# Optimization experiments

Measured on AMD Instinct MI355X. Metric: run time of the kernel, lower is better.

Reference implementation:

```python
import jax, jax.numpy as jnp
import numpy as np

ALPHA = 0.9  # membrane leak / decay


def setup_inputs() -> dict:
    key = jax.random.key(0)
    ks = jax.random.split(key, 6)
    T, B, D, H = 512, 64, 256, 256
    inputs = jax.random.normal(ks[0], (T, B, D), dtype=jnp.float32)
    spike0 = jax.random.uniform(ks[1], (B, H), dtype=jnp.float32)  # initial state['spike']
    v0 = jnp.zeros((B, H), dtype=jnp.float32)                      # initial membrane potential
    W_in = jax.random.normal(ks[2], (D, H), dtype=jnp.float32) * (1.0 / np.sqrt(D))
    W_rec = jax.random.normal(ks[3], (H, H), dtype=jnp.float32) * (1.0 / np.sqrt(H))
    W_out = jax.random.normal(ks[4], (H, H), dtype=jnp.float32) * (1.0 / np.sqrt(H))
    b = jnp.zeros((H,), dtype=jnp.float32)
    return {"inputs": inputs, "spike0": spike0, "v0": v0,
            "W_in": W_in, "W_rec": W_rec, "W_out": W_out, "b": b}


def reference(inputs, spike0, v0, W_in, W_rec, W_out, b):
    # RNNLayer.forward: sequential cell loop over time, stacking spike/pred/prob.
    def step(carry, x_t):
        v, s = carry  # membrane potential [B,H], previous spike [B,H]
        v = ALPHA * v + x_t @ W_in + s @ W_rec + b
        prob = jax.nn.sigmoid(v)
        spike = prob  # rate-coded (expected) spike
        pred = spike @ W_out
        return (v, spike), (spike, pred, prob)

    (v_T, s_T), (spikes, preds, probs) = jax.lax.scan(step, (v0, spike0), inputs)
    # torch version prepends the initial state spike: spikes has length T+1
    spikes = jnp.concatenate([spike0[None], spikes], axis=0)  # [T+1,B,H]
    return spikes, preds, probs, v_T, s_T
```

## Files before the change

kernel.cpp:

```cpp
#include <hip/hip_runtime.h>

using u16 = unsigned short;
using f32x4 = __attribute__((ext_vector_type(4))) float;
using s16x8 = __attribute__((ext_vector_type(8))) short;
using u32x4 = __attribute__((ext_vector_type(4))) unsigned int;

#define TT 512
#define BB 64
#define ALPHA 0.9f
#define SPIKES_OFF 0L
#define PREDS_OFF  8404992L
#define PROBS_OFF  16793600L
#define VT_OFF     25182208L
#define ST_OFF     25198592L

__device__ __forceinline__ u16 f2bf(float f) {
    union { float f; unsigned int i; } cv; cv.f = f;
    unsigned int x = cv.i;
    return (u16)((x + 0x7FFFu + ((x >> 16) & 1u)) >> 16);
}

__device__ __forceinline__ unsigned int cvt_pk_bf16(float lo, float hi) {
    unsigned int r;
    asm("v_cvt_pk_bf16_f32 %0, %1, %2" : "=v"(r) : "v"(lo), "v"(hi));
    return r;
}

__device__ __forceinline__ void lds_barrier() {
    __asm__ volatile("s_waitcnt lgkmcnt(0)\n\ts_barrier" ::: "memory");
}

__global__ void transpose_w(const float* __restrict__ W_in,
                            const float* __restrict__ W_rec,
                            const float* __restrict__ W_out,
                            u16* __restrict__ WT)
{
    const float* src = (blockIdx.x == 0) ? W_in : (blockIdx.x == 1) ? W_rec : W_out;
    u16* dst = WT + (long)blockIdx.x * 65536;
    const int n = threadIdx.x;
    for (int k0 = 0; k0 < 256; k0 += 8) {
        unsigned int dw[4];
        #pragma unroll
        for (int j = 0; j < 4; ++j)
            dw[j] = cvt_pk_bf16(src[(k0 + 2*j)*256 + n], src[(k0 + 2*j + 1)*256 + n]);
        u32x4 val = { dw[0], dw[1], dw[2], dw[3] };
        *(u32x4*)&dst[n*256 + k0] = val;
    }
}

template <bool ADD_BIAS, bool COPY_A>
__global__ __launch_bounds__(256, 2)
void gemm_rows(const float* __restrict__ A, const u16* __restrict__ WT,
               const float* __restrict__ bias, float* __restrict__ C,
               float* __restrict__ copyDst)
{
    const int tid  = threadIdx.x;
    const int lane = tid & 63;
    const int wave = tid >> 6;
    const int l15  = lane & 15;
    const int quad = lane >> 4;
    const long mblock = (long)blockIdx.x * 64;

    __shared__ u16 Alds[64][264];

    #pragma unroll
    for (int i = 0; i < 16; ++i) {
        int q = i*256 + tid;
        int r = q >> 6;
        int c = (q & 63) << 2;
        f32x4 a4 = *(const f32x4*)&A[(mblock + r)*256 + c];
        if (COPY_A)
            *(f32x4*)&copyDst[(mblock + r)*256 + c] = a4;
        uint2 val;
        val.x = cvt_pk_bf16(a4[0], a4[1]);
        val.y = cvt_pk_bf16(a4[2], a4[3]);
        *(uint2*)&Alds[r][c] = val;
    }

    s16x8 wfrag[4][8];
    const int nbase = wave * 64;
    #pragma unroll
    for (int nt = 0; nt < 4; ++nt)
        #pragma unroll
        for (int kt = 0; kt < 8; ++kt)
            wfrag[nt][kt] = *(const s16x8*)&WT[(nbase + nt*16 + l15)*256 + kt*32 + quad*8];

    __syncthreads();

    f32x4 acc[4][4] = {};
    #pragma unroll
    for (int kt = 0; kt < 8; ++kt) {
        s16x8 xfrag[4];
        #pragma unroll
        for (int mt = 0; mt < 4; ++mt)
            xfrag[mt] = *(const s16x8*)&Alds[mt*16 + l15][kt*32 + quad*8];
        #pragma unroll
        for (int mt = 0; mt < 4; ++mt)
            #pragma unroll
            for (int nt = 0; nt < 4; ++nt)
                acc[mt][nt] = __builtin_amdgcn_mfma_f32_16x16x32_bf16(
                    wfrag[nt][kt], xfrag[mt], acc[mt][nt], 0, 0, 0);
    }

    #pragma unroll
    for (int mt = 0; mt < 4; ++mt) {
        long m = mblock + mt*16 + l15;
        #pragma unroll
        for (int nt = 0; nt < 4; ++nt) {
            int n = nbase + nt*16 + quad*4;
            f32x4 r = acc[mt][nt];
            if (ADD_BIAS) {
                f32x4 bb = *(const f32x4*)&bias[n];
                r[0] += bb[0]; r[1] += bb[1]; r[2] += bb[2]; r[3] += bb[3];
            }
            *(f32x4*)&C[m*256 + n] = r;
        }
    }
}

__global__ __launch_bounds__(512, 2)
void recurrence_mfma(const float* __restrict__ Xin, const float* __restrict__ spike0,
                     const float* __restrict__ v0, const u16* __restrict__ WTrec,
                     float* __restrict__ out)
{
    const int tid  = threadIdx.x;
    const int lane = tid & 63;
    const int wave = tid >> 6;
    const int l15  = lane & 15;
    const int quad = lane >> 4;
    const int B0   = blockIdx.x * 16;
    const int nbase = wave * 32;
    const int hq = quad * 4;

    __shared__ u16 s_lds[2 * 16 * 256];

    const int wxor = l15 & 7;
    const int rowb = l15 * 256;
    int rOff[8];
    #pragma unroll
    for (int kt = 0; kt < 8; ++kt)
        rOff[kt] = rowb + (((kt*4 + quad) ^ wxor) << 3);
    int wOff[2];
    #pragma unroll
    for (int nt = 0; nt < 2; ++nt)
        wOff[nt] = rowb + ((((nbase >> 3) + nt*2 + (quad >> 1)) ^ wxor) << 3)
                        + ((quad & 1) << 2);

    s16x8 wfrag[2][8];
    #pragma unroll
    for (int nt = 0; nt < 2; ++nt)
        #pragma unroll
        for (int kt = 0; kt < 8; ++kt)
            wfrag[nt][kt] = *(const s16x8*)&WTrec[(nbase + nt*16 + l15)*256 + kt*32 + quad*8];

    #pragma unroll
    for (int i = 0; i < 8; ++i) {
        int idx = i*512 + tid;
        int m = idx >> 8, h = idx & 255;
        float s0v = spike0[(B0 + m)*256 + h];
        out[SPIKES_OFF + (B0 + m)*256 + h] = s0v;
        s_lds[m*256 + (((h >> 3) ^ (m & 7)) << 3) + (h & 7)] = f2bf(s0v);
    }

    const long lrow = (long)(B0 + l15) * 256;
    f32x4 v[2], xinA[2], xinB[2];
    #pragma unroll
    for (int nt = 0; nt < 2; ++nt) {
        const int h = nbase + nt*16 + hq;
        v[nt]    = *(const f32x4*)&v0[lrow + h];
        xinA[nt] = *(const f32x4*)&Xin[lrow + h];
        xinB[nt] = *(const f32x4*)&Xin[16384 + lrow + h];
    }
    const float* xin_p = Xin + 2L*16384 + lrow + nbase + hq;
    float*       pr_p  = out + PROBS_OFF + lrow + nbase + hq;

    __syncthreads();

    #pragma unroll 1
    for (int t2 = 0; t2 < TT; t2 += 2) {
        #pragma unroll
        for (int half = 0; half < 2; ++half) {
            const int rb = half, wb = half ^ 1;

            f32x4 xnew[2];
            #pragma unroll
            for (int nt = 0; nt < 2; ++nt)
                xnew[nt] = *(const f32x4*)&xin_p[nt*16];

            s16x8 sfrag[8];
            #pragma unroll
            for (int kt = 0; kt < 8; ++kt)
                sfrag[kt] = *(const s16x8*)(s_lds + (rb << 12) + rOff[kt]);

            f32x4 acc[2];
            #pragma unroll
            for (int nt = 0; nt < 2; ++nt)
                #pragma unroll
                for (int c = 0; c < 4; ++c)
                    acc[nt][c] = fmaf(ALPHA, v[nt][c],
                                      half == 0 ? xinA[nt][c] : xinB[nt][c]);
            #pragma unroll
            for (int nt = 0; nt < 2; ++nt) {
                if (half == 0) xinA[nt] = xnew[nt]; else xinB[nt] = xnew[nt];
            }

            #pragma unroll
            for (int kt = 0; kt < 8; ++kt)
                #pragma unroll
                for (int nt = 0; nt < 2; ++nt)
                    acc[nt] = __builtin_amdgcn_mfma_f32_16x16x32_bf16(
                        wfrag[nt][kt], sfrag[kt], acc[nt], 0, 0, 0);

            f32x4 p[2];
            #pragma unroll
            for (int nt = 0; nt < 2; ++nt) {
                #pragma unroll
                for (int c = 0; c < 4; ++c)
                    p[nt][c] = __builtin_amdgcn_rcpf(1.0f + __expf(-acc[nt][c]));
                uint2 sw;
                sw.x = cvt_pk_bf16(p[nt][0], p[nt][1]);
                sw.y = cvt_pk_bf16(p[nt][2], p[nt][3]);
                *(uint2*)(s_lds + (wb << 12) + wOff[nt]) = sw;
            }
            #pragma unroll
            for (int nt = 0; nt < 2; ++nt) {
                v[nt] = acc[nt];
                *(f32x4*)&pr_p[nt*16] = p[nt];
            }
            xin_p += 16384;
            pr_p  += 16384;
            lds_barrier();
        }
    }

    #pragma unroll
    for (int nt = 0; nt < 2; ++nt) {
        const int h = nbase + nt*16 + hq;
        f32x4 vv = v[nt], p;
        #pragma unroll
        for (int c = 0; c < 4; ++c)
            p[c] = __builtin_amdgcn_rcpf(1.0f + __expf(-vv[c]));
        *(f32x4*)&out[VT_OFF + lrow + h] = vv;
        *(f32x4*)&out[ST_OFF + lrow + h] = p;
    }
}

extern "C" void kernel_launch(void* const* d_in, const int* in_sizes, int n_in,
                              void* d_out, int out_size, void* d_ws, size_t ws_size,
                              hipStream_t stream) {
    const float* inputs = (const float*)d_in[0];
    const float* spike0 = (const float*)d_in[1];
    const float* v0     = (const float*)d_in[2];
    const float* W_in   = (const float*)d_in[3];
    const float* W_rec  = (const float*)d_in[4];
    const float* W_out  = (const float*)d_in[5];
    const float* bvec   = (const float*)d_in[6];
    float* out = (float*)d_out;

    u16* WT = (u16*)d_ws;
    u16* WTin  = WT;
    u16* WTrec = WT + 65536;
    u16* WTout = WT + 131072;

    float* Xin = out + PREDS_OFF;

    transpose_w<<<3, 256, 0, stream>>>(W_in, W_rec, W_out, WT);
    gemm_rows<true, false><<<512, 256, 0, stream>>>(inputs, WTin, bvec, Xin, nullptr);
    recurrence_mfma<<<4, 512, 0, stream>>>(Xin, spike0, v0, WTrec, out);
    gemm_rows<false, true><<<512, 256, 0, stream>>>(out + PROBS_OFF, WTout, bvec,
                                                    out + PREDS_OFF, out + 16384);
}
```

Baseline: 555.3 us.

## Replace per-step block barrier with per-wave LDS flags for fine-grained dataflow sync

```diff
diff --git a/kernel.cpp b/kernel.cpp
--- a/kernel.cpp
+++ b/kernel.cpp
@@ -26,8 +26,10 @@
     return r;
 }
 
-__device__ __forceinline__ void lds_barrier() {
-    __asm__ volatile("s_waitcnt lgkmcnt(0)\n\ts_barrier" ::: "memory");
+__device__ __forceinline__ unsigned and0(unsigned x) {
+    unsigned r;
+    asm("v_and_b32 %0, 0, %1" : "=v"(r) : "v"(x));
+    return r;
 }
 
 __global__ void transpose_w(const float* __restrict__ W_in,
@@ -133,26 +135,31 @@
     const int hq = quad * 4;
 
     __shared__ u16 s_lds[2 * 16 * 256];
+    __shared__ __align__(16) unsigned s_flags[2][8];
 
     const int wxor = l15 & 7;
     const int rowb = l15 * 256;
-    int rOff[8];
-    #pragma unroll
-    for (int kt = 0; kt < 8; ++kt)
-        rOff[kt] = rowb + (((kt*4 + quad) ^ wxor) << 3);
+
+    int ktR[8], rOffR[8];
+    #pragma unroll
+    for (int i = 0; i < 8; ++i) {
+        ktR[i] = (wave + i) & 7;
+        rOffR[i] = rowb + (((ktR[i]*4 + quad) ^ wxor) << 3);
+    }
     int wOff[2];
     #pragma unroll
     for (int nt = 0; nt < 2; ++nt)
         wOff[nt] = rowb + ((((nbase >> 3) + nt*2 + (quad >> 1)) ^ wxor) << 3)
                         + ((quad & 1) << 2);
 
-    s16x8 wfrag[2][8];
-    #pragma unroll
-    for (int nt = 0; nt < 2; ++nt)
-        #pragma unroll
-        for (int kt = 0; kt < 8; ++kt)
-            wfrag[nt][kt] = *(const s16x8*)&WTrec[(nbase + nt*16 + l15)*256 + kt*32 + quad*8];
-
+    s16x8 wfragR[2][8];
+    #pragma unroll
+    for (int i = 0; i < 8; ++i)
+        #pragma unroll
+        for (int nt = 0; nt < 2; ++nt)
+            wfragR[nt][i] = *(const s16x8*)&WTrec[(nbase + nt*16 + l15)*256 + ktR[i]*32 + quad*8];
+
+    if (tid < 16) ((unsigned*)s_flags)[tid] = 0u;
     #pragma unroll
     for (int i = 0; i < 8; ++i) {
         int idx = i*512 + tid;
@@ -176,21 +183,40 @@
 
     __syncthreads();
 
+#define GET_SLICE(i_)                                                         \
+    if (!((rdy >> ktR[i_]) & 1)) {                                            \
+        volatile unsigned* f_ = (volatile unsigned*)&s_flags[rb][ktR[i_]];    \
+        unsigned fv_; do { fv_ = *f_; } while (fv_ != want);                  \
+        z += and0(fv_);                                                       \
+    }                                                                         \
+    sfrag[i_] = *(const s16x8*)(s_lds + ldsbase + rOffR[i_] + z);
+
+#define DO_MFMA(i_)                                                           \
+    acc[0] = __builtin_amdgcn_mfma_f32_16x16x32_bf16(wfragR[0][i_], sfrag[i_], acc[0], 0, 0, 0); \
+    acc[1] = __builtin_amdgcn_mfma_f32_16x16x32_bf16(wfragR[1][i_], sfrag[i_], acc[1], 0, 0, 0);
+
     #pragma unroll 1
     for (int t2 = 0; t2 < TT; t2 += 2) {
         #pragma unroll
         for (int half = 0; half < 2; ++half) {
             const int rb = half, wb = half ^ 1;
+            const int ldsbase = rb << 12;
+            const unsigned want = (unsigned)(t2 + half);
 
             f32x4 xnew[2];
-            #pragma unroll
-            for (int nt = 0; nt < 2; ++nt)
-                xnew[nt] = *(const f32x4*)&xin_p[nt*16];
+            xnew[0] = *(const f32x4*)&xin_p[0];
+            xnew[1] = *(const f32x4*)&xin_p[16];
 
             s16x8 sfrag[8];
-            #pragma unroll
-            for (int kt = 0; kt < 8; ++kt)
-                sfrag[kt] = *(const s16x8*)(s_lds + (rb << 12) + rOff[kt]);
+            sfrag[0] = *(const s16x8*)(s_lds + ldsbase + rOffR[0]);
+
+            u32x4 snA = *(const u32x4*)&s_flags[rb][0];
+            u32x4 snB = *(const u32x4*)&s_flags[rb][4];
+            unsigned rdy = (snA[0] == want ?   1u : 0u) | (snA[1] == want ?   2u : 0u)
+                         | (snA[2] == want ?   4u : 0u) | (snA[3] == want ?   8u : 0u)
+                         | (snB[0] == want ?  16u : 0u) | (snB[1] == want ?  32u : 0u)
+                         | (snB[2] == want ?  64u : 0u) | (snB[3] == want ? 128u : 0u);
+            unsigned z = and0(rdy);
 
             f32x4 acc[2];
             #pragma unroll
@@ -204,12 +230,14 @@
                 if (half == 0) xinA[nt] = xnew[nt]; else xinB[nt] = xnew[nt];
             }
 
-            #pragma unroll
-            for (int kt = 0; kt < 8; ++kt)
-                #pragma unroll
-                for (int nt = 0; nt < 2; ++nt)
-                    acc[nt] = __builtin_amdgcn_mfma_f32_16x16x32_bf16(
-                        wfrag[nt][kt], sfrag[kt], acc[nt], 0, 0, 0);
+            GET_SLICE(1); GET_SLICE(2);
+            DO_MFMA(0);
+            GET_SLICE(3); DO_MFMA(1);
+            GET_SLICE(4); DO_MFMA(2);
+            GET_SLICE(5); DO_MFMA(3);
+            GET_SLICE(6); DO_MFMA(4);
+            GET_SLICE(7); DO_MFMA(5);
+            DO_MFMA(6);   DO_MFMA(7);
 
             f32x4 p[2];
             #pragma unroll
@@ -222,6 +250,10 @@
                 sw.y = cvt_pk_bf16(p[nt][2], p[nt][3]);
                 *(uint2*)(s_lds + (wb << 12) + wOff[nt]) = sw;
             }
+            asm volatile("s_waitcnt lgkmcnt(0)" ::: "memory");
+            if (lane == 0)
+                *(volatile unsigned*)&s_flags[wb][wave] = want + 1;
+
             #pragma unroll
             for (int nt = 0; nt < 2; ++nt) {
                 v[nt] = acc[nt];
@@ -229,9 +261,10 @@
             }
             xin_p += 16384;
             pr_p  += 16384;
-            lds_barrier();
         }
     }
+#undef GET_SLICE
+#undef DO_MFMA
 
     #pragma unroll
     for (int nt = 0; nt < 2; ++nt) {
```

Result: slower. 685.4 us (+23.4%).

## Split recurrent MFMA chain into two accumulators and deepen Xin prefetch

Applied to the files above, without the earlier changes.

```diff
diff --git a/kernel.cpp b/kernel.cpp
--- a/kernel.cpp
+++ b/kernel.cpp
@@ -163,72 +163,97 @@
     }
 
     const long lrow = (long)(B0 + l15) * 256;
-    f32x4 v[2], xinA[2], xinB[2];
+    const int  lvo  = (int)lrow + nbase + hq;
+
+    f32x4 Astate[2], vfin[2], xq[4][2];
+    #pragma unroll
+    for (int slot = 0; slot < 4; ++slot)
+        #pragma unroll
+        for (int nt = 0; nt < 2; ++nt)
+            xq[slot][nt] = *(const f32x4*)&Xin[(unsigned)(slot*16384 + lvo) + nt*16];
     #pragma unroll
     for (int nt = 0; nt < 2; ++nt) {
-        const int h = nbase + nt*16 + hq;
-        v[nt]    = *(const f32x4*)&v0[lrow + h];
-        xinA[nt] = *(const f32x4*)&Xin[lrow + h];
-        xinB[nt] = *(const f32x4*)&Xin[16384 + lrow + h];
-    }
-    const float* xin_p = Xin + 2L*16384 + lrow + nbase + hq;
-    float*       pr_p  = out + PROBS_OFF + lrow + nbase + hq;
+        f32x4 vv = *(const f32x4*)&v0[lrow + nbase + nt*16 + hq];
+        #pragma unroll
+        for (int c = 0; c < 4; ++c)
+            Astate[nt][c] = fmaf(ALPHA, vv[c], xq[0][nt][c]);
+    }
+    const f32x4 z4 = { 0.0f, 0.0f, 0.0f, 0.0f };
+
+    unsigned xoff = (unsigned)(4*16384 + lvo);
+    unsigned poff = (unsigned)lvo;
+    const float* probs_base = out + PROBS_OFF;
 
     __syncthreads();
 
     #pragma unroll 1
-    for (int t2 = 0; t2 < TT; t2 += 2) {
-        #pragma unroll
-        for (int half = 0; half < 2; ++half) {
-            const int rb = half, wb = half ^ 1;
+    for (int t4 = 0; t4 < TT; t4 += 4) {
+        #pragma unroll
+        for (int half = 0; half < 4; ++half) {
+            const int rb = half & 1, wb = rb ^ 1;
+            const int ldsbase = rb << 12;
 
             f32x4 xnew[2];
+            xnew[0] = *(const f32x4*)&Xin[xoff];
+            xnew[1] = *(const f32x4*)&Xin[xoff + 16];
+
+            s16x8 sfrag[8];
+            sfrag[0] = *(const s16x8*)(s_lds + ldsbase + rOff[0]);
+            sfrag[4] = *(const s16x8*)(s_lds + ldsbase + rOff[4]);
+            sfrag[1] = *(const s16x8*)(s_lds + ldsbase + rOff[1]);
+            sfrag[5] = *(const s16x8*)(s_lds + ldsbase + rOff[5]);
+            sfrag[2] = *(const s16x8*)(s_lds + ldsbase + rOff[2]);
+            sfrag[6] = *(const s16x8*)(s_lds + ldsbase + rOff[6]);
+            sfrag[3] = *(const s16x8*)(s_lds + ldsbase + rOff[3]);
+            sfrag[7] = *(const s16x8*)(s_lds + ldsbase + rOff[7]);
+
+            f32x4 AL[2], AH[2];
+            #pragma unroll
+            for (int nt = 0; nt < 2; ++nt) {
+                AL[nt] = __builtin_amdgcn_mfma_f32_16x16x32_bf16(
+                             wfrag[nt][0], sfrag[0], Astate[nt], 0, 0, 0);
+                AH[nt] = __builtin_amdgcn_mfma_f32_16x16x32_bf16(
+                             wfrag[nt][4], sfrag[4], z4, 0, 0, 0);
+            }
+            #pragma unroll
+            for (int k = 1; k < 4; ++k)
+                #pragma unroll
+                for (int nt = 0; nt < 2; ++nt) {
+                    AL[nt] = __builtin_amdgcn_mfma_f32_16x16x32_bf16(
+                                 wfrag[nt][k], sfrag[k], AL[nt], 0, 0, 0);
+                    AH[nt] = __builtin_amdgcn_mfma_f32_16x16x32_bf16(
+                                 wfrag[nt][k+4], sfrag[k+4], AH[nt], 0, 0, 0);
+                }
             #pragma unroll
             for (int nt = 0; nt < 2; ++nt)
-                xnew[nt] = *(const f32x4*)&xin_p[nt*16];
-
-            s16x8 sfrag[8];
-            #pragma unroll
-            for (int kt = 0; kt < 8; ++kt)
-                sfrag[kt] = *(const s16x8*)(s_lds + (rb << 12) + rOff[kt]);
-
-            f32x4 acc[2];
-            #pragma unroll
-            for (int nt = 0; nt < 2; ++nt)
                 #pragma unroll
                 for (int c = 0; c < 4; ++c)
-                    acc[nt][c] = fmaf(ALPHA, v[nt][c],
-                                      half == 0 ? xinA[nt][c] : xinB[nt][c]);
+                    vfin[nt][c] = AL[nt][c] + AH[nt][c];
+
             #pragma unroll
             for (int nt = 0; nt < 2; ++nt) {
-                if (half == 0) xinA[nt] = xnew[nt]; else xinB[nt] = xnew[nt];
-            }
-
-            #pragma unroll
-            for (int kt = 0; kt < 8; ++kt)
-                #pragma unroll
-                for (int nt = 0; nt < 2; ++nt)
-                    acc[nt] = __builtin_amdgcn_mfma_f32_16x16x32_bf16(
-                        wfrag[nt][kt], sfrag[kt], acc[nt], 0, 0, 0);
+                const int nslot = (half + 1) & 3;
+                #pragma unroll
+                for (int c = 0; c < 4; ++c)
+                    Astate[nt][c] = fmaf(ALPHA, vfin[nt][c], xq[nslot][nt][c]);
+                xq[half][nt] = xnew[nt];
+            }
 
             f32x4 p[2];
             #pragma unroll
             for (int nt = 0; nt < 2; ++nt) {
                 #pragma unroll
                 for (int c = 0; c < 4; ++c)
-                    p[nt][c] = __builtin_amdgcn_rcpf(1.0f + __expf(-acc[nt][c]));
+                    p[nt][c] = __builtin_amdgcn_rcpf(1.0f + __expf(-vfin[nt][c]));
                 uint2 sw;
                 sw.x = cvt_pk_bf16(p[nt][0], p[nt][1]);
                 sw.y = cvt_pk_bf16(p[nt][2], p[nt][3]);
                 *(uint2*)(s_lds + (wb << 12) + wOff[nt]) = sw;
             }
-            #pragma unroll
-            for (int nt = 0; nt < 2; ++nt) {
-                v[nt] = acc[nt];
-                *(f32x4*)&pr_p[nt*16] = p[nt];
-            }
-            xin_p += 16384;
-            pr_p  += 16384;
+            *(f32x4*)&probs_base[poff]      = p[0];
+            *(f32x4*)&probs_base[poff + 16] = p[1];
+            xoff += 16384;
+            poff += 16384;
             lds_barrier();
         }
     }
@@ -236,7 +261,7 @@
     #pragma unroll
     for (int nt = 0; nt < 2; ++nt) {
         const int h = nbase + nt*16 + hq;
-        f32x4 vv = v[nt], p;
+        f32x4 vv = vfin[nt], p;
         #pragma unroll
         for (int c = 0; c < 4; ++c)
             p[c] = __builtin_amdgcn_rcpf(1.0f + __expf(-vv[c]));
```

Result: no change. 557.4 us (+0.4%).

## Fuse output projection into recurrence kernel and drop separate pred GEMM

Applied to the files above, without the earlier changes.

```diff
diff --git a/kernel.cpp b/kernel.cpp
--- a/kernel.cpp
+++ b/kernel.cpp
@@ -48,11 +48,10 @@
     }
 }
 
-template <bool ADD_BIAS, bool COPY_A>
+template <bool ADD_BIAS>
 __global__ __launch_bounds__(256, 2)
 void gemm_rows(const float* __restrict__ A, const u16* __restrict__ WT,
-               const float* __restrict__ bias, float* __restrict__ C,
-               float* __restrict__ copyDst)
+               const float* __restrict__ bias, float* __restrict__ C)
 {
     const int tid  = threadIdx.x;
     const int lane = tid & 63;
@@ -69,8 +68,6 @@
         int r = q >> 6;
         int c = (q & 63) << 2;
         f32x4 a4 = *(const f32x4*)&A[(mblock + r)*256 + c];
-        if (COPY_A)
-            *(f32x4*)&copyDst[(mblock + r)*256 + c] = a4;
         uint2 val;
         val.x = cvt_pk_bf16(a4[0], a4[1]);
         val.y = cvt_pk_bf16(a4[2], a4[3]);
@@ -121,7 +118,7 @@
 __global__ __launch_bounds__(512, 2)
 void recurrence_mfma(const float* __restrict__ Xin, const float* __restrict__ spike0,
                      const float* __restrict__ v0, const u16* __restrict__ WTrec,
-                     float* __restrict__ out)
+                     const u16* __restrict__ WTout, float* __restrict__ out)
 {
     const int tid  = threadIdx.x;
     const int lane = tid & 63;
@@ -146,12 +143,14 @@
         wOff[nt] = rowb + ((((nbase >> 3) + nt*2 + (quad >> 1)) ^ wxor) << 3)
                         + ((quad & 1) << 2);
 
-    s16x8 wfrag[2][8];
+    s16x8 wfrag[2][8], wfragOut[2][8];
     #pragma unroll
     for (int nt = 0; nt < 2; ++nt)
         #pragma unroll
-        for (int kt = 0; kt < 8; ++kt)
-            wfrag[nt][kt] = *(const s16x8*)&WTrec[(nbase + nt*16 + l15)*256 + kt*32 + quad*8];
+        for (int kt = 0; kt < 8; ++kt) {
+            wfrag[nt][kt]    = *(const s16x8*)&WTrec[(nbase + nt*16 + l15)*256 + kt*32 + quad*8];
+            wfragOut[nt][kt] = *(const s16x8*)&WTout[(nbase + nt*16 + l15)*256 + kt*32 + quad*8];
+        }
 
     #pragma unroll
     for (int i = 0; i < 8; ++i) {
@@ -163,6 +162,7 @@
     }
 
     const long lrow = (long)(B0 + l15) * 256;
+    const unsigned lvo = (unsigned)lrow + nbase + hq;
     f32x4 v[2], xinA[2], xinB[2];
     #pragma unroll
     for (int nt = 0; nt < 2; ++nt) {
@@ -171,8 +171,11 @@
         xinA[nt] = *(const f32x4*)&Xin[lrow + h];
         xinB[nt] = *(const f32x4*)&Xin[16384 + lrow + h];
     }
-    const float* xin_p = Xin + 2L*16384 + lrow + nbase + hq;
-    float*       pr_p  = out + PROBS_OFF + lrow + nbase + hq;
+    const float* xin_p = Xin + 2L*16384 + lvo;
+    unsigned pr_off = (unsigned)PROBS_OFF + lvo;
+    unsigned sp_off = 16384u + lvo;
+    unsigned pd_off = (unsigned)VT_OFF + lvo;
+    const f32x4 z4 = { 0.0f, 0.0f, 0.0f, 0.0f };
 
     __syncthreads();
 
@@ -181,16 +184,16 @@
         #pragma unroll
         for (int half = 0; half < 2; ++half) {
             const int rb = half, wb = half ^ 1;
+            const int ldsbase = rb << 12;
 
             f32x4 xnew[2];
-            #pragma unroll
-            for (int nt = 0; nt < 2; ++nt)
-                xnew[nt] = *(const f32x4*)&xin_p[nt*16];
+            xnew[0] = *(const f32x4*)&xin_p[0];
+            xnew[1] = *(const f32x4*)&xin_p[16];
 
             s16x8 sfrag[8];
             #pragma unroll
             for (int kt = 0; kt < 8; ++kt)
-                sfrag[kt] = *(const s16x8*)(s_lds + (rb << 12) + rOff[kt]);
+                sfrag[kt] = *(const s16x8*)(s_lds + ldsbase + rOff[kt]);
 
             f32x4 acc[2];
             #pragma unroll
@@ -222,15 +225,52 @@
                 sw.y = cvt_pk_bf16(p[nt][2], p[nt][3]);
                 *(uint2*)(s_lds + (wb << 12) + wOff[nt]) = sw;
             }
-            #pragma unroll
-            for (int nt = 0; nt < 2; ++nt) {
+
+            f32x4 accP0, accP1;
+            accP0 = __builtin_amdgcn_mfma_f32_16x16x32_bf16(
+                        wfragOut[0][0], sfrag[0], z4, 0, 0, 0);
+            accP1 = __builtin_amdgcn_mfma_f32_16x16x32_bf16(
+                        wfragOut[1][0], sfrag[0], z4, 0, 0, 0);
+            #pragma unroll
+            for (int kt = 1; kt < 8; ++kt) {
+                accP0 = __builtin_amdgcn_mfma_f32_16x16x32_bf16(
+                            wfragOut[0][kt], sfrag[kt], accP0, 0, 0, 0);
+                accP1 = __builtin_amdgcn_mfma_f32_16x16x32_bf16(
+                            wfragOut[1][kt], sfrag[kt], accP1, 0, 0, 0);
+            }
+
+            #pragma unroll
+            for (int nt = 0; nt < 2; ++nt)
                 v[nt] = acc[nt];
-                *(f32x4*)&pr_p[nt*16] = p[nt];
-            }
-            xin_p += 16384;
-            pr_p  += 16384;
+            *(f32x4*)&out[pr_off]      = p[0];
+            *(f32x4*)&out[pr_off + 16] = p[1];
+            *(f32x4*)&out[sp_off]      = p[0];
+            *(f32x4*)&out[sp_off + 16] = p[1];
+            *(f32x4*)&out[pd_off]      = accP0;
+            *(f32x4*)&out[pd_off + 16] = accP1;
+            pd_off = sp_off + (unsigned)(PREDS_OFF - 16384);
+            pr_off += 16384;
+            sp_off += 16384;
+            xin_p  += 16384;
             lds_barrier();
         }
+    }
+
+    {
+        s16x8 sf[8];
+        #pragma unroll
+        for (int kt = 0; kt < 8; ++kt)
+            sf[kt] = *(const s16x8*)(s_lds + rOff[kt]);
+        f32x4 aP0, aP1;
+        aP0 = __builtin_amdgcn_mfma_f32_16x16x32_bf16(wfragOut[0][0], sf[0], z4, 0, 0, 0);
+        aP1 = __builtin_amdgcn_mfma_f32_16x16x32_bf16(wfragOut[1][0], sf[0], z4, 0, 0, 0);
+        #pragma unroll
+        for (int kt = 1; kt < 8; ++kt) {
+            aP0 = __builtin_amdgcn_mfma_f32_16x16x32_bf16(wfragOut[0][kt], sf[kt], aP0, 0, 0, 0);
+            aP1 = __builtin_amdgcn_mfma_f32_16x16x32_bf16(wfragOut[1][kt], sf[kt], aP1, 0, 0, 0);
+        }
+        *(f32x4*)&out[pd_off]      = aP0;
+        *(f32x4*)&out[pd_off + 16] = aP1;
     }
 
     #pragma unroll
@@ -265,8 +305,6 @@
     float* Xin = out + PREDS_OFF;
 
     transpose_w<<<3, 256, 0, stream>>>(W_in, W_rec, W_out, WT);
-    gemm_rows<true, false><<<512, 256, 0, stream>>>(inputs, WTin, bvec, Xin, nullptr);
-    recurrence_mfma<<<4, 512, 0, stream>>>(Xin, spike0, v0, WTrec, out);
-    gemm_rows<false, true><<<512, 256, 0, stream>>>(out + PROBS_OFF, WTout, bvec,
-                                                    out + PREDS_OFF, out + 16384);
-}
+    gemm_rows<true><<<512, 256, 0, stream>>>(inputs, WTin, bvec, Xin);
+    recurrence_mfma<<<4, 512, 0, stream>>>(Xin, spike0, v0, WTrec, WTout, out);
+}
```

Result: slower. 1.045 ms (+88.2%).
